# Kernel optimization log

Measured on AMD Instinct MI355X. Metric: run time of the kernel, lower is better.

The kernel has to match this reference:

```python
import jax, jax.numpy as jnp
import numpy as np

N = 50000
E = 500000
HID = 64
HEADS = 4
LAYERS = 4
CDIM = 8


def _p(key, shape, scale=0.05):
    return jax.random.normal(key, shape, dtype=jnp.float32) * scale


def setup_inputs() -> dict:
    key = jax.random.key(0)
    ks = jax.random.split(key, 32)
    x = jax.random.normal(ks[0], (N, 8), dtype=jnp.float32)
    src = jax.random.randint(ks[1], (E,), 0, N)
    dst = jax.random.randint(ks[2], (E,), 0, N)
    edge_index = jnp.stack([src, dst]).astype(jnp.int64)
    HC = HEADS * HID
    inp = {
        "x": x,
        "edge_index": edge_index,
        # encoder: Linear(8,64), ELU, Linear(64,64), ELU
        "enc_w1": _p(ks[3], (HID, 8)), "enc_b1": _p(ks[4], (HID,)),
        "enc_w2": _p(ks[5], (HID, HID)), "enc_b2": _p(ks[6], (HID,)),
        # per-layer TransformerConv params, stacked over layers
        "Wq": _p(ks[7], (LAYERS, HC, HID)), "bq": _p(ks[8], (LAYERS, HC)),
        "Wk": _p(ks[9], (LAYERS, HC, HID)), "bk": _p(ks[10], (LAYERS, HC)),
        "Wv": _p(ks[11], (LAYERS, HC, HID)), "bv": _p(ks[12], (LAYERS, HC)),
        "Ws": _p(ks[13], (LAYERS, HID, HID)), "bs": _p(ks[14], (LAYERS, HID)),
        # output MLP: 64->64->32->8
        "out_w1": _p(ks[15], (64, HID)), "out_b1": _p(ks[16], (64,)),
        "out_w2": _p(ks[17], (32, 64)), "out_b2": _p(ks[18], (32,)),
        "out_w3": _p(ks[19], (CDIM, 32)), "out_b3": _p(ks[20], (CDIM,)),
    }
    return inp


def transformer_conv(h, src, dst, Wq, bq, Wk, bk, Wv, bv, Ws, bs):
    """PyG TransformerConv, concat=False, root_weight=True, eval mode (no dropout)."""
    n = h.shape[0]
    q = (h @ Wq.T + bq).reshape(n, HEADS, HID)
    k = (h @ Wk.T + bk).reshape(n, HEADS, HID)
    v = (h @ Wv.T + bv).reshape(n, HEADS, HID)
    # per-edge multi-head scores: (E, H)
    alpha = jnp.einsum("ehd,ehd->eh", q[dst], k[src]) / np.sqrt(HID).astype(np.float32)
    # segment softmax over edges grouped by destination node
    amax = jax.ops.segment_max(alpha, dst, num_segments=n)          # (N, H)
    ex = jnp.exp(alpha - amax[dst])                                 # (E, H)
    denom = jax.ops.segment_sum(ex, dst, num_segments=n)           # (N, H)
    w = ex / denom[dst]                                             # (E, H)
    msg = v[src] * w[:, :, None]                                    # (E, H, C)
    agg = jax.ops.segment_sum(msg, dst, num_segments=n)            # (N, H, C)
    out = agg.mean(axis=1)                                          # concat=False -> head mean
    return out + h @ Ws.T + bs                                      # skip connection


def reference(x, edge_index, enc_w1, enc_b1, enc_w2, enc_b2,
              Wq, bq, Wk, bk, Wv, bv, Ws, bs,
              out_w1, out_b1, out_w2, out_b2, out_w3, out_b3):
    src, dst = edge_index[0], edge_index[1]
    elu = jax.nn.elu
    h = elu(x @ enc_w1.T + enc_b1)
    h = elu(h @ enc_w2.T + enc_b2)
    for l in range(LAYERS):
        h = elu(transformer_conv(h, src, dst, Wq[l], bq[l], Wk[l], bk[l],
                                 Wv[l], bv[l], Ws[l], bs[l]))
        # dropout is identity in eval mode
    o = elu(h @ out_w1.T + out_b1)
    o = elu(o @ out_w2.T + out_b2)
    o = o @ out_w3.T + out_b3
    return o
```

## Files before the change

### kernel.cpp

```cpp
#include <hip/hip_runtime.h>
#include <hip/hip_bf16.h>

#define N_NODES 50000
#define N_EDGES 500000
constexpr int HID = 64;
constexpr int HC  = 256;

typedef unsigned short u16;
typedef unsigned char u8;
typedef __attribute__((ext_vector_type(8))) __bf16 bf16x8;
typedef __attribute__((ext_vector_type(4))) float f32x4;
typedef __attribute__((ext_vector_type(2))) float f32x2;

__device__ __forceinline__ float b2f(u16 u) {
    union { unsigned int i; float f; } c; c.i = ((unsigned int)u) << 16; return c.f;
}
__device__ __forceinline__ u16 f2b(float f) {
    union { float f; unsigned int i; } c; c.f = f;
    unsigned int x = c.i;
    unsigned int lsb = (x >> 16) & 1u;
    x += 0x7fffu + lsb;
    return (u16)(x >> 16);
}
__device__ __forceinline__ float elu_f(float x) { return x > 0.f ? x : expm1f(x); }


__global__ __launch_bounds__(256) void init_kernel(int* __restrict__ cnt, int* __restrict__ cursor) {
    int i = blockIdx.x * 256 + threadIdx.x;
    if (i < N_NODES) { cnt[i] = 0; cursor[i] = 0; }
}

__global__ __launch_bounds__(256) void detect_kernel(const int* __restrict__ ei, int* __restrict__ flag) {
    __shared__ int s[4];
    int t = threadIdx.x;
    int nz = ei[2 * t + 1] != 0;
    unsigned long long m = __ballot(nz);
    if ((t & 63) == 0) s[t >> 6] = (m != 0ull) ? 1 : 0;
    __syncthreads();
    if (t == 0) flag[0] = s[0] | s[1] | s[2] | s[3];
}

__global__ __launch_bounds__(256) void wcvt_kernel(const float* __restrict__ Wq, const float* __restrict__ Wk,
                                                   const float* __restrict__ Wv, const float* __restrict__ Wsk,
                                                   u16* __restrict__ w16) {
    int i = blockIdx.x * 256 + threadIdx.x;
    if (i >= 53248) return;
    const float* src; int off;
    if (i < 16384)      { src = Wq;  off = i; }
    else if (i < 32768) { src = Wk;  off = i - 16384; }
    else if (i < 49152) { src = Wv;  off = i - 32768; }
    else                { src = Wsk; off = i - 49152; }
    float4 v = ((const float4*)src)[off];
    ushort4 u; u.x = f2b(v.x); u.y = f2b(v.y); u.z = f2b(v.z); u.w = f2b(v.w);
    ((ushort4*)w16)[i] = u;
}

__global__ __launch_bounds__(256) void hist_kernel(const int* __restrict__ ei, const int* __restrict__ flag,
                                                   int* __restrict__ cnt) {
    int e = blockIdx.x * 256 + threadIdx.x;
    if (e < N_EDGES) {
        int d = flag[0] ? ei[N_EDGES + e] : ei[2 * N_EDGES + 2 * e];
        atomicAdd(&cnt[d], 1);
    }
}

__global__ __launch_bounds__(512) void scan1_kernel(const int* __restrict__ cnt,
                                                    int* __restrict__ row_start, int* __restrict__ bsum) {
    __shared__ int sc[512];
    int t = threadIdx.x;
    int i = blockIdx.x * 512 + t;
    int v = (i < N_NODES) ? cnt[i] : 0;
    sc[t] = v;
    __syncthreads();
    for (int off = 1; off < 512; off <<= 1) {
        int u = (t >= off) ? sc[t - off] : 0;
        __syncthreads();
        sc[t] += u;
        __syncthreads();
    }
    if (i < N_NODES) row_start[i] = sc[t] - v;
    if (t == 511) bsum[blockIdx.x] = sc[511];
}

__global__ __launch_bounds__(128) void scan2_kernel(int* __restrict__ bsum, int* __restrict__ row_start) {
    __shared__ int sc[128];
    const int NB = (N_NODES + 511) / 512;
    int t = threadIdx.x;
    int v = (t < NB) ? bsum[t] : 0;
    sc[t] = v;
    __syncthreads();
    for (int off = 1; off < 128; off <<= 1) {
        int u = (t >= off) ? sc[t - off] : 0;
        __syncthreads();
        sc[t] += u;
        __syncthreads();
    }
    if (t < NB) bsum[t] = sc[t] - v;
    if (t == 127) row_start[N_NODES] = sc[127];
}

__global__ __launch_bounds__(512) void scan3_kernel(int* __restrict__ row_start, const int* __restrict__ bsum) {
    int i = blockIdx.x * 512 + threadIdx.x;
    if (i < N_NODES) row_start[i] += bsum[blockIdx.x];
}

__global__ __launch_bounds__(256) void scatter_kernel(const int* __restrict__ ei, const int* __restrict__ flag,
                                const int* __restrict__ row_start, int* __restrict__ cursor,
                                int* __restrict__ csr_src) {
    int e = blockIdx.x * 256 + threadIdx.x;
    if (e < N_EDGES) {
        int isI32 = flag[0];
        int s = isI32 ? ei[e] : ei[2 * e];
        int d = isI32 ? ei[N_EDGES + e] : ei[2 * N_EDGES + 2 * e];
        int pos = row_start[d] + atomicAdd(&cursor[d], 1);
        csr_src[pos] = s;
    }
}

__global__ __launch_bounds__(256) void encoder_kernel(const float* __restrict__ x,
                               const float* __restrict__ w1, const float* __restrict__ b1,
                               const float* __restrict__ w2, const float* __restrict__ b2,
                               float* __restrict__ h) {
    __shared__ float xs[64 * 9];
    __shared__ float w1s[64 * 9];
    __shared__ u16 t1s[64 * 72];
    __shared__ u16 w2s[64 * 72];
    __shared__ float b1s[64], b2s[64];
    int t = threadIdx.x;
    int m0 = blockIdx.x * 64;

    if (t < 128) {
        int row = t >> 1, c = (t & 1) * 4;
        float4 val = make_float4(0.f, 0.f, 0.f, 0.f);
        if (m0 + row < N_NODES) val = *(const float4*)(x + (size_t)(m0 + row) * 8 + c);
        *(float4*)&xs[row * 9 + c] = val;
    }
    if (t >= 128 && t < 256) {
        int p = t - 128;
        int row = p >> 1, c = (p & 1) * 4;
        float4 val = *(const float4*)(w1 + row * 8 + c);
        *(float4*)&w1s[row * 9 + c] = val;
    }
    #pragma unroll
    for (int r = 0; r < 4; ++r) {
        int p = t + r * 256; int row = p >> 4, kc = (p & 15) * 4;
        float4 val = *(const float4*)(w2 + row * 64 + kc);
        ushort4 u; u.x = f2b(val.x); u.y = f2b(val.y); u.z = f2b(val.z); u.w = f2b(val.w);
        *(ushort4*)&w2s[row * 72 + kc] = u;
    }
    if (t < 64) { b1s[t] = b1[t]; b2s[t] = b2[t]; }
    __syncthreads();

    {
        int j = t & 63, sub = t >> 6;
        #pragma unroll
        for (int g = 0; g < 16; ++g) {
            int node = g * 4 + sub;
            float acc = b1s[j];
            #pragma unroll
            for (int m = 0; m < 8; ++m) acc += xs[node * 9 + m] * w1s[j * 9 + m];
            t1s[node * 72 + j] = f2b(elu_f(acc));
        }
    }
    __syncthreads();

    int wave = t >> 6, lane = t & 63;
    int lrow = lane & 15, quad = lane >> 4;
    int m_off = wave * 16;
    bf16x8 a0 = *(const bf16x8*)&t1s[(m_off + lrow) * 72 + quad * 8];
    bf16x8 a1 = *(const bf16x8*)&t1s[(m_off + lrow) * 72 + 32 + quad * 8];
    #pragma unroll
    for (int nsub = 0; nsub < 4; ++nsub) {
        bf16x8 b0 = *(const bf16x8*)&w2s[(nsub * 16 + lrow) * 72 + quad * 8];
        bf16x8 b1v = *(const bf16x8*)&w2s[(nsub * 16 + lrow) * 72 + 32 + quad * 8];
        f32x4 acc = {0.f, 0.f, 0.f, 0.f};
        acc = __builtin_amdgcn_mfma_f32_16x16x32_bf16(a0, b0, acc, 0, 0, 0);
        acc = __builtin_amdgcn_mfma_f32_16x16x32_bf16(a1, b1v, acc, 0, 0, 0);
        int col = nsub * 16 + lrow;
        float bias = b2s[col];
        #pragma unroll
        for (int r = 0; r < 4; ++r) {
            int row = m0 + m_off + quad * 4 + r;
            if (row < N_NODES) h[(size_t)row * 64 + col] = elu_f(acc[r] + bias);
        }
    }
}

__global__ __launch_bounds__(256) void proj_kernel(const float* __restrict__ h,
    const u16* __restrict__ wq16, const u16* __restrict__ wk16,
    const u16* __restrict__ wv16, const u16* __restrict__ wsk16,
    const float* __restrict__ bq, const float* __restrict__ bk,
    const float* __restrict__ bv, const float* __restrict__ bsk,
    int layer,
    u16* __restrict__ q, u8* __restrict__ kv, float* __restrict__ skip)
{
    __shared__ u16 as_tile[64 * 72];
    __shared__ u16 ws_tile[64 * 72];
    __shared__ float pool[64 * 68];
    u16* qst  = (u16*)pool;
    u8*  kvst = (u8*)pool;
    float* skst = pool;

    int t = threadIdx.x;
    int m0 = blockIdx.x * 64;

    #pragma unroll
    for (int r = 0; r < 4; ++r) {
        int p = t + r * 256; int row = p >> 4, kc = (p & 15) * 4;
        float4 val = make_float4(0.f, 0.f, 0.f, 0.f);
        if (m0 + row < N_NODES) val = *(const float4*)(h + (size_t)(m0 + row) * 64 + kc);
        ushort4 u; u.x = f2b(val.x); u.y = f2b(val.y); u.z = f2b(val.z); u.w = f2b(val.w);
        *(ushort4*)&as_tile[row * 72 + kc] = u;
    }
    __syncthreads();

    int wave = t >> 6, lane = t & 63;
    int lrow = lane & 15, quad = lane >> 4;
    bf16x8 a0 = *(const bf16x8*)&as_tile[(wave * 16 + lrow) * 72 + quad * 8];
    bf16x8 a1 = *(const bf16x8*)&as_tile[(wave * 16 + lrow) * 72 + 32 + quad * 8];

    const u16* Wq16  = wq16  + (size_t)layer * HC * HID;
    const u16* Wk16  = wk16  + (size_t)layer * HC * HID;
    const u16* Wv16  = wv16  + (size_t)layer * HC * HID;
    const u16* Wsk16 = wsk16 + (size_t)layer * HID * HID;
    const float* bqL  = bq  + layer * HC;
    const float* bkL  = bk  + layer * HC;
    const float* bvL  = bv  + layer * HC;
    const float* bskL = bsk + layer * HID;

    int nl = wave * 16 + lrow;

    for (int ct = 0; ct < 4; ++ct) {
        int cbase = ct * 64;
        __syncthreads();
        #pragma unroll
        for (int it = 0; it < 2; ++it) {
            int p = t + it * 256; int row = p >> 3, kc = (p & 7) * 8;
            *(uint4*)&ws_tile[row * 72 + kc] = *(const uint4*)(Wq16 + (size_t)(cbase + row) * 64 + kc);
        }
        __syncthreads();
        #pragma unroll
        for (int nsub = 0; nsub < 4; ++nsub) {
            bf16x8 w0 = *(const bf16x8*)&ws_tile[(nsub * 16 + lrow) * 72 + quad * 8];
            bf16x8 w1 = *(const bf16x8*)&ws_tile[(nsub * 16 + lrow) * 72 + 32 + quad * 8];
            f32x4 acc = {0.f, 0.f, 0.f, 0.f};
            acc = __builtin_amdgcn_mfma_f32_16x16x32_bf16(w0, a0, acc, 0, 0, 0);
            acc = __builtin_amdgcn_mfma_f32_16x16x32_bf16(w1, a1, acc, 0, 0, 0);
            float4 b4 = *(const float4*)(bqL + cbase + nsub * 16 + quad * 4);
            ushort4 o;
            o.x = f2b(acc[0] + b4.x); o.y = f2b(acc[1] + b4.y);
            o.z = f2b(acc[2] + b4.z); o.w = f2b(acc[3] + b4.w);
            *(ushort4*)&qst[nl * 72 + nsub * 16 + quad * 4] = o;
        }
        __syncthreads();
        #pragma unroll
        for (int it = 0; it < 2; ++it) {
            int p = t + it * 256; int row = p >> 3, ch = p & 7;
            int grow = m0 + row;
            if (grow < N_NODES)
                *(uint4*)(q + (size_t)grow * 256 + cbase + ch * 8) = *(const uint4*)&qst[row * 72 + ch * 8];
        }
    }

    for (int ct = 0; ct < 4; ++ct) {
        int cbase = ct * 64;
        __syncthreads();
        #pragma unroll
        for (int it = 0; it < 2; ++it) {
            int p = t + it * 256; int row = p >> 3, kc = (p & 7) * 8;
            *(uint4*)&ws_tile[row * 72 + kc] = *(const uint4*)(Wk16 + (size_t)(cbase + row) * 64 + kc);
        }
        __syncthreads();
        #pragma unroll
        for (int nsub = 0; nsub < 4; ++nsub) {
            bf16x8 w0 = *(const bf16x8*)&ws_tile[(nsub * 16 + lrow) * 72 + quad * 8];
            bf16x8 w1 = *(const bf16x8*)&ws_tile[(nsub * 16 + lrow) * 72 + 32 + quad * 8];
            f32x4 acc = {0.f, 0.f, 0.f, 0.f};
            acc = __builtin_amdgcn_mfma_f32_16x16x32_bf16(w0, a0, acc, 0, 0, 0);
            acc = __builtin_amdgcn_mfma_f32_16x16x32_bf16(w1, a1, acc, 0, 0, 0);
            float4 b4 = *(const float4*)(bkL + cbase + nsub * 16 + quad * 4);
            float f0 = (acc[0] + b4.x) * 16.f, f1 = (acc[1] + b4.y) * 16.f;
            float f2v = (acc[2] + b4.z) * 16.f, f3v = (acc[3] + b4.w) * 16.f;
            int pk = __builtin_amdgcn_cvt_pk_fp8_f32(f0, f1, 0, false);
            pk = __builtin_amdgcn_cvt_pk_fp8_f32(f2v, f3v, pk, true);
            int g = nsub * 4 + quad;
            *(unsigned int*)&kvst[nl * 144 + g * 8] = (unsigned int)pk;
        }
        __syncthreads();
        #pragma unroll
        for (int it = 0; it < 2; ++it) {
            int p = t + it * 256; int row = p >> 3, kc = (p & 7) * 8;
            *(uint4*)&ws_tile[row * 72 + kc] = *(const uint4*)(Wv16 + (size_t)(cbase + row) * 64 + kc);
        }
        __syncthreads();
        #pragma unroll
        for (int nsub = 0; nsub < 4; ++nsub) {
            bf16x8 w0 = *(const bf16x8*)&ws_tile[(nsub * 16 + lrow) * 72 + quad * 8];
            bf16x8 w1 = *(const bf16x8*)&ws_tile[(nsub * 16 + lrow) * 72 + 32 + quad * 8];
            f32x4 acc = {0.f, 0.f, 0.f, 0.f};
            acc = __builtin_amdgcn_mfma_f32_16x16x32_bf16(w0, a0, acc, 0, 0, 0);
            acc = __builtin_amdgcn_mfma_f32_16x16x32_bf16(w1, a1, acc, 0, 0, 0);
            float4 b4 = *(const float4*)(bvL + cbase + nsub * 16 + quad * 4);
            float f0 = (acc[0] + b4.x) * 16.f, f1 = (acc[1] + b4.y) * 16.f;
            float f2v = (acc[2] + b4.z) * 16.f, f3v = (acc[3] + b4.w) * 16.f;
            int pk = __builtin_amdgcn_cvt_pk_fp8_f32(f0, f1, 0, false);
            pk = __builtin_amdgcn_cvt_pk_fp8_f32(f2v, f3v, pk, true);
            int g = nsub * 4 + quad;
            *(unsigned int*)&kvst[nl * 144 + g * 8 + 4] = (unsigned int)pk;
        }
        __syncthreads();
        #pragma unroll
        for (int it = 0; it < 2; ++it) {
            int p = t + it * 256; int row = p >> 3, ch = p & 7;
            int grow = m0 + row;
            if (grow < N_NODES)
                *(uint4*)(kv + (size_t)grow * 512 + cbase * 2 + ch * 16) = *(const uint4*)&kvst[row * 144 + ch * 16];
        }
    }

    {
        __syncthreads();
        #pragma unroll
        for (int it = 0; it < 2; ++it) {
            int p = t + it * 256; int row = p >> 3, kc = (p & 7) * 8;
            *(uint4*)&ws_tile[row * 72 + kc] = *(const uint4*)(Wsk16 + (size_t)row * 64 + kc);
        }
        __syncthreads();
        #pragma unroll
        for (int nsub = 0; nsub < 4; ++nsub) {
            bf16x8 w0 = *(const bf16x8*)&ws_tile[(nsub * 16 + lrow) * 72 + quad * 8];
            bf16x8 w1 = *(const bf16x8*)&ws_tile[(nsub * 16 + lrow) * 72 + 32 + quad * 8];
            f32x4 acc = {0.f, 0.f, 0.f, 0.f};
            acc = __builtin_amdgcn_mfma_f32_16x16x32_bf16(w0, a0, acc, 0, 0, 0);
            acc = __builtin_amdgcn_mfma_f32_16x16x32_bf16(w1, a1, acc, 0, 0, 0);
            float4 b4 = *(const float4*)(bskL + nsub * 16 + quad * 4);
            float4 o;
            o.x = acc[0] + b4.x; o.y = acc[1] + b4.y;
            o.z = acc[2] + b4.z; o.w = acc[3] + b4.w;
            *(float4*)&skst[nl * 68 + nsub * 16 + quad * 4] = o;
        }
        __syncthreads();
        int row = t >> 2, c0 = (t & 3) * 16;
        int grow = m0 + row;
        if (grow < N_NODES) {
            #pragma unroll
            for (int j = 0; j < 4; ++j)
                *(float4*)(skip + (size_t)grow * 64 + c0 + j * 4) = *(const float4*)&skst[row * 68 + c0 + j * 4];
        }
    }
}

#define ATTN_QUAD(S0q, S1q, S2q, S3q, V1, V2, V3) do { \
    uint2 c0 = *(const uint2*)(kvl + (size_t)(unsigned)(S0q) * 512); \
    uint2 c1 = *(const uint2*)(kvl + (size_t)(unsigned)(S1q) * 512); \
    uint2 c2 = *(const uint2*)(kvl + (size_t)(unsigned)(S2q) * 512); \
    uint2 c3 = *(const uint2*)(kvl + (size_t)(unsigned)(S3q) * 512); \
    f32x2 k0a = __builtin_amdgcn_cvt_pk_f32_fp8(c0.x, false), k0b = __builtin_amdgcn_cvt_pk_f32_fp8(c0.x, true); \
    f32x2 k1a = __builtin_amdgcn_cvt_pk_f32_fp8(c1.x, false), k1b = __builtin_amdgcn_cvt_pk_f32_fp8(c1.x, true); \
    f32x2 k2a = __builtin_amdgcn_cvt_pk_f32_fp8(c2.x, false), k2b = __builtin_amdgcn_cvt_pk_f32_fp8(c2.x, true); \
    f32x2 k3a = __builtin_amdgcn_cvt_pk_f32_fp8(c3.x, false), k3b = __builtin_amdgcn_cvt_pk_f32_fp8(c3.x, true); \
    f32x2 pd0 = qlo * k0a + qhi * k0b; \
    f32x2 pd1 = qlo * k1a + qhi * k1b; \
    f32x2 pd2 = qlo * k2a + qhi * k2b; \
    f32x2 pd3 = qlo * k3a + qhi * k3b; \
    float p0 = pd0.x + pd0.y, p1 = pd1.x + pd1.y, p2 = pd2.x + pd2.y, p3 = pd3.x + pd3.y; \
    p0 += __shfl_xor(p0, 1); p1 += __shfl_xor(p1, 1); p2 += __shfl_xor(p2, 1); p3 += __shfl_xor(p3, 1); \
    p0 += __shfl_xor(p0, 2); p1 += __shfl_xor(p1, 2); p2 += __shfl_xor(p2, 2); p3 += __shfl_xor(p3, 2); \
    p0 += __shfl_xor(p0, 4); p1 += __shfl_xor(p1, 4); p2 += __shfl_xor(p2, 4); p3 += __shfl_xor(p3, 4); \
    p0 += __shfl_xor(p0, 8); p1 += __shfl_xor(p1, 8); p2 += __shfl_xor(p2, 8); p3 += __shfl_xor(p3, 8); \
    float w0 = __expf(p0 * SC); \
    float w1 = (V1) ? __expf(p1 * SC) : 0.f; \
    float w2 = (V2) ? __expf(p2 * SC) : 0.f; \
    float w3 = (V3) ? __expf(p3 * SC) : 0.f; \
    l += (w0 + w1) + (w2 + w3); \
    f32x2 v0a = __builtin_amdgcn_cvt_pk_f32_fp8(c0.y, false), v0b = __builtin_amdgcn_cvt_pk_f32_fp8(c0.y, true); \
    f32x2 v1a = __builtin_amdgcn_cvt_pk_f32_fp8(c1.y, false), v1b = __builtin_amdgcn_cvt_pk_f32_fp8(c1.y, true); \
    f32x2 v2a = __builtin_amdgcn_cvt_pk_f32_fp8(c2.y, false), v2b = __builtin_amdgcn_cvt_pk_f32_fp8(c2.y, true); \
    f32x2 v3a = __builtin_amdgcn_cvt_pk_f32_fp8(c3.y, false), v3b = __builtin_amdgcn_cvt_pk_f32_fp8(c3.y, true); \
    accA += v0a * w0; accA += v1a * w1; accA += v2a * w2; accA += v3a * w3; \
    accB += v0b * w0; accB += v1b * w1; accB += v2b * w2; accB += v3b * w3; \
} while (0)

__global__ __launch_bounds__(256) void attn_kernel(
    const u16* __restrict__ q, const u8* __restrict__ kv,
    const float* __restrict__ skip,
    const int* __restrict__ row_start, const int* __restrict__ csr_src,
    float* __restrict__ hout)
{
    __shared__ int s_lds[4][64];
    int wave = threadIdx.x >> 6;
    int lane = threadIdx.x & 63;
    int n = blockIdx.x * 4 + wave;
    if (n >= N_NODES) return;
    ushort4 q4 = ((const ushort4*)(q + (size_t)n * 256))[lane];
    f32x2 qlo = { b2f(q4.x), b2f(q4.y) };
    f32x2 qhi = { b2f(q4.z), b2f(q4.w) };
    const u8* kvl = kv + lane * 8;
    const float SC = 0.0078125f;
    float l = 0.f;
    f32x2 accA = {0.f, 0.f};
    f32x2 accB = {0.f, 0.f};
    int e0 = row_start[n];
    int deg = row_start[n + 1] - e0;

    for (int base = 0; base < deg; base += 64) {
        int rem = deg - base;
        int m = rem < 64 ? rem : 64;
        int li = lane < m ? lane : m - 1;
        s_lds[wave][lane] = csr_src[e0 + base + li];
        int i = 0;
        for (; i + 4 <= m; i += 4) {
            int4 sq = *(const int4*)&s_lds[wave][i];
            ATTN_QUAD(sq.x, sq.y, sq.z, sq.w, 1, 1, 1);
        }
        if (i < m) {
            int4 sq = *(const int4*)&s_lds[wave][i];
            int rem2 = m - i;
            int sB = rem2 > 1 ? sq.y : sq.x;
            int sC = rem2 > 2 ? sq.z : sq.x;
            ATTN_QUAD(sq.x, sB, sC, sq.x, rem2 > 1, rem2 > 2, 0);
        }
    }

    float inv = l > 0.f ? 1.f / l : 0.f;
    float a0 = accA.x * inv, a1 = accA.y * inv;
    float a2 = accB.x * inv, a3 = accB.y * inv;
    a0 += __shfl_xor(a0, 16); a0 += __shfl_xor(a0, 32);
    a1 += __shfl_xor(a1, 16); a1 += __shfl_xor(a1, 32);
    a2 += __shfl_xor(a2, 16); a2 += __shfl_xor(a2, 32);
    a3 += __shfl_xor(a3, 16); a3 += __shfl_xor(a3, 32);
    if ((lane >> 4) == 0) {
        const float OS = 0.015625f;
        float4 sk = ((const float4*)(skip + (size_t)n * 64))[lane];
        float4 o;
        o.x = elu_f(OS * a0 + sk.x);
        o.y = elu_f(OS * a1 + sk.y);
        o.z = elu_f(OS * a2 + sk.z);
        o.w = elu_f(OS * a3 + sk.w);
        ((float4*)(hout + (size_t)n * 64))[lane] = o;
    }
}

__global__ __launch_bounds__(256) void mlp_kernel(const float* __restrict__ h,
    const float* __restrict__ w1, const float* __restrict__ b1,
    const float* __restrict__ w2, const float* __restrict__ b2,
    const float* __restrict__ w3, const float* __restrict__ b3,
    float* __restrict__ out)
{
    __shared__ u16 hs[64 * 72];
    __shared__ u16 w1s[64 * 72];
    __shared__ u16 t1s[64 * 72];
    __shared__ u16 w2s[32 * 72];
    __shared__ float t2s[64 * 33];
    __shared__ float w3s[8 * 33];
    __shared__ float b1s[64], b2s[32], b3s[8];
    int t = threadIdx.x;
    int m0 = blockIdx.x * 64;

    #pragma unroll
    for (int r = 0; r < 4; ++r) {
        int p = t + r * 256; int row = p >> 4, kc = (p & 15) * 4;
        float4 val = make_float4(0.f, 0.f, 0.f, 0.f);
        if (m0 + row < N_NODES) val = *(const float4*)(h + (size_t)(m0 + row) * 64 + kc);
        ushort4 u; u.x = f2b(val.x); u.y = f2b(val.y); u.z = f2b(val.z); u.w = f2b(val.w);
        *(ushort4*)&hs[row * 72 + kc] = u;
    }
    #pragma unroll
    for (int r = 0; r < 4; ++r) {
        int p = t + r * 256; int row = p >> 4, kc = (p & 15) * 4;
        float4 val = *(const float4*)(w1 + row * 64 + kc);
        ushort4 u; u.x = f2b(val.x); u.y = f2b(val.y); u.z = f2b(val.z); u.w = f2b(val.w);
        *(ushort4*)&w1s[row * 72 + kc] = u;
    }
    #pragma unroll
    for (int r = 0; r < 2; ++r) {
        int p = t + r * 256; int row = p >> 4, kc = (p & 15) * 4;
        float4 val = *(const float4*)(w2 + row * 64 + kc);
        ushort4 u; u.x = f2b(val.x); u.y = f2b(val.y); u.z = f2b(val.z); u.w = f2b(val.w);
        *(ushort4*)&w2s[row * 72 + kc] = u;
    }
    if (t < 8 * 32) { int r = t >> 5, c = t & 31; w3s[r * 33 + c] = w3[t]; }
    if (t < 64) b1s[t] = b1[t];
    if (t >= 64 && t < 96) b2s[t - 64] = b2[t - 64];
    if (t >= 96 && t < 104) b3s[t - 96] = b3[t - 96];
    __syncthreads();

    int wave = t >> 6, lane = t & 63;
    int lrow = lane & 15, quad = lane >> 4;
    int m_off = wave * 16;

    {
        bf16x8 a0 = *(const bf16x8*)&hs[(m_off + lrow) * 72 + quad * 8];
        bf16x8 a1 = *(const bf16x8*)&hs[(m_off + lrow) * 72 + 32 + quad * 8];
        #pragma unroll
        for (int nsub = 0; nsub < 4; ++nsub) {
            bf16x8 b0 = *(const bf16x8*)&w1s[(nsub * 16 + lrow) * 72 + quad * 8];
            bf16x8 b1v = *(const bf16x8*)&w1s[(nsub * 16 + lrow) * 72 + 32 + quad * 8];
            f32x4 acc = {0.f, 0.f, 0.f, 0.f};
            acc = __builtin_amdgcn_mfma_f32_16x16x32_bf16(a0, b0, acc, 0, 0, 0);
            acc = __builtin_amdgcn_mfma_f32_16x16x32_bf16(a1, b1v, acc, 0, 0, 0);
            int col = nsub * 16 + lrow;
            float bias = b1s[col];
            #pragma unroll
            for (int r = 0; r < 4; ++r) {
                int row = m_off + quad * 4 + r;
                t1s[row * 72 + col] = f2b(elu_f(acc[r] + bias));
            }
        }
    }
    __syncthreads();

    {
        bf16x8 a0 = *(const bf16x8*)&t1s[(m_off + lrow) * 72 + quad * 8];
        bf16x8 a1 = *(const bf16x8*)&t1s[(m_off + lrow) * 72 + 32 + quad * 8];
        #pragma unroll
        for (int nsub = 0; nsub < 2; ++nsub) {
            bf16x8 b0 = *(const bf16x8*)&w2s[(nsub * 16 + lrow) * 72 + quad * 8];
            bf16x8 b1v = *(const bf16x8*)&w2s[(nsub * 16 + lrow) * 72 + 32 + quad * 8];
            f32x4 acc = {0.f, 0.f, 0.f, 0.f};
            acc = __builtin_amdgcn_mfma_f32_16x16x32_bf16(a0, b0, acc, 0, 0, 0);
            acc = __builtin_amdgcn_mfma_f32_16x16x32_bf16(a1, b1v, acc, 0, 0, 0);
            int col = nsub * 16 + lrow;
            float bias = b2s[col];
            #pragma unroll
            for (int r = 0; r < 4; ++r) {
                int row = m_off + quad * 4 + r;
                t2s[row * 33 + col] = elu_f(acc[r] + bias);
            }
        }
    }
    __syncthreads();

    #pragma unroll
    for (int r = 0; r < 2; ++r) {
        int idx = t + r * 256;
        int node = idx >> 3, j = idx & 7;
        int row = m0 + node;
        if (row < N_NODES) {
            float acc = b3s[j];
            #pragma unroll
            for (int kk = 0; kk < 32; ++kk) acc += t2s[node * 33 + kk] * w3s[j * 33 + kk];
            out[(size_t)row * 8 + j] = acc;
        }
    }
}

extern "C" void kernel_launch(void* const* d_in, const int* in_sizes, int n_in,
                              void* d_out, int out_size, void* d_ws, size_t ws_size,
                              hipStream_t stream) {
    (void)in_sizes; (void)n_in; (void)out_size; (void)ws_size;
    const float* x   = (const float*)d_in[0];
    const int* ei    = (const int*)d_in[1];
    const float* ew1 = (const float*)d_in[2];
    const float* eb1 = (const float*)d_in[3];
    const float* ew2 = (const float*)d_in[4];
    const float* eb2 = (const float*)d_in[5];
    const float* Wq  = (const float*)d_in[6];
    const float* bq  = (const float*)d_in[7];
    const float* Wk  = (const float*)d_in[8];
    const float* bk  = (const float*)d_in[9];
    const float* Wv  = (const float*)d_in[10];
    const float* bv  = (const float*)d_in[11];
    const float* Wsk = (const float*)d_in[12];
    const float* bsk = (const float*)d_in[13];
    const float* ow1 = (const float*)d_in[14];
    const float* ob1 = (const float*)d_in[15];
    const float* ow2 = (const float*)d_in[16];
    const float* ob2 = (const float*)d_in[17];
    const float* ow3 = (const float*)d_in[18];
    const float* ob3 = (const float*)d_in[19];

    char* ws = (char*)d_ws;
    size_t off = 0;
    auto alloc = [&](size_t bytes) -> void* {
        void* p = ws + off;
        off += (bytes + 255) & ~(size_t)255;
        return p;
    };
    float* h0    = (float*)alloc((size_t)N_NODES * 64 * 4);
    float* h1    = (float*)alloc((size_t)N_NODES * 64 * 4);
    u16*   q     = (u16*)  alloc((size_t)N_NODES * 256 * 2);
    u8*    kv    = (u8*)   alloc((size_t)N_NODES * 512);
    float* skp   = (float*)alloc((size_t)N_NODES * 64 * 4);
    u16*   w16   = (u16*)  alloc((size_t)212992 * 2);
    int*   cnt   = (int*)  alloc((size_t)N_NODES * 4);
    int*   cursor= (int*)  alloc((size_t)N_NODES * 4);
    int*   rowst = (int*)  alloc((size_t)(N_NODES + 1) * 4);
    int*   csr   = (int*)  alloc((size_t)N_EDGES * 4);
    int*   bsum  = (int*)  alloc(512);
    int*   flag  = (int*)  alloc(256);

    u16* wq16  = w16;
    u16* wk16  = w16 + 65536;
    u16* wv16  = w16 + 131072;
    u16* wsk16 = w16 + 196608;

    const int NB = (N_NODES + 511) / 512;

    init_kernel<<<(N_NODES + 255) / 256, 256, 0, stream>>>(cnt, cursor);
    detect_kernel<<<1, 256, 0, stream>>>(ei, flag);
    wcvt_kernel<<<208, 256, 0, stream>>>(Wq, Wk, Wv, Wsk, w16);
    hist_kernel<<<(N_EDGES + 255) / 256, 256, 0, stream>>>(ei, flag, cnt);
    scan1_kernel<<<NB, 512, 0, stream>>>(cnt, rowst, bsum);
    scan2_kernel<<<1, 128, 0, stream>>>(bsum, rowst);
    scan3_kernel<<<NB, 512, 0, stream>>>(rowst, bsum);
    scatter_kernel<<<(N_EDGES + 255) / 256, 256, 0, stream>>>(ei, flag, rowst, cursor, csr);

    encoder_kernel<<<(N_NODES + 63) / 64, 256, 0, stream>>>(x, ew1, eb1, ew2, eb2, h0);

    float* hin = h0;
    float* hout = h1;
    for (int l = 0; l < 4; ++l) {
        proj_kernel<<<(N_NODES + 63) / 64, 256, 0, stream>>>(hin, wq16, wk16, wv16, wsk16,
                                                             bq, bk, bv, bsk, l, q, kv, skp);
        attn_kernel<<<(N_NODES + 3) / 4, 256, 0, stream>>>(q, kv, skp, rowst, csr, hout);
        float* tmp = hin; hin = hout; hout = tmp;
    }

    mlp_kernel<<<(N_NODES + 63) / 64, 256, 0, stream>>>(hin, ow1, ob1, ow2, ob2, ow3, ob3, (float*)d_out);
}
```

Measured before the change: 470.6 us.

## Store hidden states as bf16, unroll attention gather by eight, memset counters

The hidden-state buffers between layers change from fp32 to bf16. The encoder and attention kernels now write bf16, and the projection and MLP kernels load it directly instead of converting on load, which halves that traffic. The attention edge loop issues eight KV gathers before computing, to expose more memory-level parallelism. The init kernel is replaced by a single hipMemsetAsync over the contiguous cnt and cursor arrays. This adds bf16 rounding of the stored activations, which were already rounded to bf16 when fed into the matmuls, and the memset relies on cursor directly following cnt in the workspace.

```diff
diff --git a/kernel.cpp b/kernel.cpp
--- a/kernel.cpp
+++ b/kernel.cpp
@@ -24,11 +24,6 @@
 }
 __device__ __forceinline__ float elu_f(float x) { return x > 0.f ? x : expm1f(x); }
 
-
-__global__ __launch_bounds__(256) void init_kernel(int* __restrict__ cnt, int* __restrict__ cursor) {
-    int i = blockIdx.x * 256 + threadIdx.x;
-    if (i < N_NODES) { cnt[i] = 0; cursor[i] = 0; }
-}
 
 __global__ __launch_bounds__(256) void detect_kernel(const int* __restrict__ ei, int* __restrict__ flag) {
     __shared__ int s[4];
@@ -120,7 +115,7 @@
 __global__ __launch_bounds__(256) void encoder_kernel(const float* __restrict__ x,
                                const float* __restrict__ w1, const float* __restrict__ b1,
                                const float* __restrict__ w2, const float* __restrict__ b2,
-                               float* __restrict__ h) {
+                               u16* __restrict__ h) {
     __shared__ float xs[64 * 9];
     __shared__ float w1s[64 * 9];
     __shared__ u16 t1s[64 * 72];
@@ -181,12 +176,12 @@
         #pragma unroll
         for (int r = 0; r < 4; ++r) {
             int row = m0 + m_off + quad * 4 + r;
-            if (row < N_NODES) h[(size_t)row * 64 + col] = elu_f(acc[r] + bias);
-        }
-    }
-}
-
-__global__ __launch_bounds__(256) void proj_kernel(const float* __restrict__ h,
+            if (row < N_NODES) h[(size_t)row * 64 + col] = f2b(elu_f(acc[r] + bias));
+        }
+    }
+}
+
+__global__ __launch_bounds__(256) void proj_kernel(const u16* __restrict__ h,
     const u16* __restrict__ wq16, const u16* __restrict__ wk16,
     const u16* __restrict__ wv16, const u16* __restrict__ wsk16,
     const float* __restrict__ bq, const float* __restrict__ bk,
@@ -205,12 +200,11 @@
     int m0 = blockIdx.x * 64;
 
     #pragma unroll
-    for (int r = 0; r < 4; ++r) {
-        int p = t + r * 256; int row = p >> 4, kc = (p & 15) * 4;
-        float4 val = make_float4(0.f, 0.f, 0.f, 0.f);
-        if (m0 + row < N_NODES) val = *(const float4*)(h + (size_t)(m0 + row) * 64 + kc);
-        ushort4 u; u.x = f2b(val.x); u.y = f2b(val.y); u.z = f2b(val.z); u.w = f2b(val.w);
-        *(ushort4*)&as_tile[row * 72 + kc] = u;
+    for (int it = 0; it < 2; ++it) {
+        int p = t + it * 256; int row = p >> 3, kc = (p & 7) * 8;
+        uint4 val = make_uint4(0u, 0u, 0u, 0u);
+        if (m0 + row < N_NODES) val = *(const uint4*)(h + (size_t)(m0 + row) * 64 + kc);
+        *(uint4*)&as_tile[row * 72 + kc] = val;
     }
     __syncthreads();
 
@@ -350,11 +344,9 @@
     }
 }
 
-#define ATTN_QUAD(S0q, S1q, S2q, S3q, V1, V2, V3) do { \
-    uint2 c0 = *(const uint2*)(kvl + (size_t)(unsigned)(S0q) * 512); \
-    uint2 c1 = *(const uint2*)(kvl + (size_t)(unsigned)(S1q) * 512); \
-    uint2 c2 = *(const uint2*)(kvl + (size_t)(unsigned)(S2q) * 512); \
-    uint2 c3 = *(const uint2*)(kvl + (size_t)(unsigned)(S3q) * 512); \
+#define KV_LOAD(cv, S) uint2 cv = *(const uint2*)(kvl + (size_t)(unsigned)(S) * 512)
+
+#define ATTN_BODY(c0, c1, c2, c3, V1, V2, V3) do { \
     f32x2 k0a = __builtin_amdgcn_cvt_pk_f32_fp8(c0.x, false), k0b = __builtin_amdgcn_cvt_pk_f32_fp8(c0.x, true); \
     f32x2 k1a = __builtin_amdgcn_cvt_pk_f32_fp8(c1.x, false), k1b = __builtin_amdgcn_cvt_pk_f32_fp8(c1.x, true); \
     f32x2 k2a = __builtin_amdgcn_cvt_pk_f32_fp8(c2.x, false), k2b = __builtin_amdgcn_cvt_pk_f32_fp8(c2.x, true); \
@@ -385,7 +377,7 @@
     const u16* __restrict__ q, const u8* __restrict__ kv,
     const float* __restrict__ skip,
     const int* __restrict__ row_start, const int* __restrict__ csr_src,
-    float* __restrict__ hout)
+    u16* __restrict__ hout)
 {
     __shared__ int s_lds[4][64];
     int wave = threadIdx.x >> 6;
@@ -409,16 +401,27 @@
         int li = lane < m ? lane : m - 1;
         s_lds[wave][lane] = csr_src[e0 + base + li];
         int i = 0;
-        for (; i + 4 <= m; i += 4) {
+        for (; i + 8 <= m; i += 8) {
+            int4 sa = *(const int4*)&s_lds[wave][i];
+            int4 sb = *(const int4*)&s_lds[wave][i + 4];
+            KV_LOAD(c0, sa.x); KV_LOAD(c1, sa.y); KV_LOAD(c2, sa.z); KV_LOAD(c3, sa.w);
+            KV_LOAD(d0, sb.x); KV_LOAD(d1, sb.y); KV_LOAD(d2, sb.z); KV_LOAD(d3, sb.w);
+            ATTN_BODY(c0, c1, c2, c3, 1, 1, 1);
+            ATTN_BODY(d0, d1, d2, d3, 1, 1, 1);
+        }
+        if (i + 4 <= m) {
             int4 sq = *(const int4*)&s_lds[wave][i];
-            ATTN_QUAD(sq.x, sq.y, sq.z, sq.w, 1, 1, 1);
+            KV_LOAD(c0, sq.x); KV_LOAD(c1, sq.y); KV_LOAD(c2, sq.z); KV_LOAD(c3, sq.w);
+            ATTN_BODY(c0, c1, c2, c3, 1, 1, 1);
+            i += 4;
         }
         if (i < m) {
             int4 sq = *(const int4*)&s_lds[wave][i];
             int rem2 = m - i;
             int sB = rem2 > 1 ? sq.y : sq.x;
             int sC = rem2 > 2 ? sq.z : sq.x;
-            ATTN_QUAD(sq.x, sB, sC, sq.x, rem2 > 1, rem2 > 2, 0);
+            KV_LOAD(c0, sq.x); KV_LOAD(c1, sB); KV_LOAD(c2, sC); KV_LOAD(c3, sq.x);
+            ATTN_BODY(c0, c1, c2, c3, rem2 > 1, rem2 > 2, 0);
         }
     }
 
@@ -432,16 +435,16 @@
     if ((lane >> 4) == 0) {
         const float OS = 0.015625f;
         float4 sk = ((const float4*)(skip + (size_t)n * 64))[lane];
-        float4 o;
-        o.x = elu_f(OS * a0 + sk.x);
-        o.y = elu_f(OS * a1 + sk.y);
-        o.z = elu_f(OS * a2 + sk.z);
-        o.w = elu_f(OS * a3 + sk.w);
-        ((float4*)(hout + (size_t)n * 64))[lane] = o;
-    }
-}
-
-__global__ __launch_bounds__(256) void mlp_kernel(const float* __restrict__ h,
+        ushort4 o;
+        o.x = f2b(elu_f(OS * a0 + sk.x));
+        o.y = f2b(elu_f(OS * a1 + sk.y));
+        o.z = f2b(elu_f(OS * a2 + sk.z));
+        o.w = f2b(elu_f(OS * a3 + sk.w));
+        ((ushort4*)(hout + (size_t)n * 64))[lane] = o;
+    }
+}
+
+__global__ __launch_bounds__(256) void mlp_kernel(const u16* __restrict__ h,
     const float* __restrict__ w1, const float* __restrict__ b1,
     const float* __restrict__ w2, const float* __restrict__ b2,
     const float* __restrict__ w3, const float* __restrict__ b3,
@@ -458,12 +461,11 @@
     int m0 = blockIdx.x * 64;
 
     #pragma unroll
-    for (int r = 0; r < 4; ++r) {
-        int p = t + r * 256; int row = p >> 4, kc = (p & 15) * 4;
-        float4 val = make_float4(0.f, 0.f, 0.f, 0.f);
-        if (m0 + row < N_NODES) val = *(const float4*)(h + (size_t)(m0 + row) * 64 + kc);
-        ushort4 u; u.x = f2b(val.x); u.y = f2b(val.y); u.z = f2b(val.z); u.w = f2b(val.w);
-        *(ushort4*)&hs[row * 72 + kc] = u;
+    for (int it = 0; it < 2; ++it) {
+        int p = t + it * 256; int row = p >> 3, kc = (p & 7) * 8;
+        uint4 val = make_uint4(0u, 0u, 0u, 0u);
+        if (m0 + row < N_NODES) val = *(const uint4*)(h + (size_t)(m0 + row) * 64 + kc);
+        *(uint4*)&hs[row * 72 + kc] = val;
     }
     #pragma unroll
     for (int r = 0; r < 4; ++r) {
@@ -577,8 +579,8 @@
         off += (bytes + 255) & ~(size_t)255;
         return p;
     };
-    float* h0    = (float*)alloc((size_t)N_NODES * 64 * 4);
-    float* h1    = (float*)alloc((size_t)N_NODES * 64 * 4);
+    u16*   h0    = (u16*)  alloc((size_t)N_NODES * 64 * 2);
+    u16*   h1    = (u16*)  alloc((size_t)N_NODES * 64 * 2);
     u16*   q     = (u16*)  alloc((size_t)N_NODES * 256 * 2);
     u8*    kv    = (u8*)   alloc((size_t)N_NODES * 512);
     float* skp   = (float*)alloc((size_t)N_NODES * 64 * 4);
@@ -597,7 +599,7 @@
 
     const int NB = (N_NODES + 511) / 512;
 
-    init_kernel<<<(N_NODES + 255) / 256, 256, 0, stream>>>(cnt, cursor);
+    hipMemsetAsync(cnt, 0, 2 * 200192, stream);
     detect_kernel<<<1, 256, 0, stream>>>(ei, flag);
     wcvt_kernel<<<208, 256, 0, stream>>>(Wq, Wk, Wv, Wsk, w16);
     hist_kernel<<<(N_EDGES + 255) / 256, 256, 0, stream>>>(ei, flag, cnt);
@@ -608,13 +610,13 @@
 
     encoder_kernel<<<(N_NODES + 63) / 64, 256, 0, stream>>>(x, ew1, eb1, ew2, eb2, h0);
 
-    float* hin = h0;
-    float* hout = h1;
+    u16* hin = h0;
+    u16* hout = h1;
     for (int l = 0; l < 4; ++l) {
         proj_kernel<<<(N_NODES + 63) / 64, 256, 0, stream>>>(hin, wq16, wk16, wv16, wsk16,
                                                              bq, bk, bv, bsk, l, q, kv, skp);
         attn_kernel<<<(N_NODES + 3) / 4, 256, 0, stream>>>(q, kv, skp, rowst, csr, hout);
-        float* tmp = hin; hin = hout; hout = tmp;
+        u16* tmp = hin; hin = hout; hout = tmp;
     }
 
     mlp_kernel<<<(N_NODES + 63) / 64, 256, 0, stream>>>(hin, ow1, ob1, ow2, ob2, ow3, ob3, (float*)d_out);
```

Measured after the change: 523.5 us. +11.2%, slower.
